# Performance work log

Measured on AMD Instinct MI355X. Metric: run time of the kernel, lower is better.

The kernel has to match this reference:

```python
import jax, jax.numpy as jnp
import numpy as np

T_STEP, NUM_PATCHES = 16, 49
DIM, MLP_DIM, HEADS, DEPTH = 512, 2048, 8, 4
PATCH_DIM = 432
N_BATCH = 32
NEG = -1e9
EPS = 1e-5


def _ln(x, g, b):
    m = x.mean(-1, keepdims=True)
    v = ((x - m) ** 2).mean(-1, keepdims=True)
    return (x - m) / jnp.sqrt(v + EPS) * g + b


def setup_inputs() -> dict:
    key = jax.random.key(0)
    ks = jax.random.split(key, 16)
    L = T_STEP * NUM_PATCHES
    s = 0.02
    return {
        "patch": jax.random.normal(ks[0], (N_BATCH, L, PATCH_DIM), jnp.float32),
        "done": jax.random.randint(ks[1], (N_BATCH, T_STEP - 1), 0, 2).astype(jnp.int32),
        "W_embed": jax.random.normal(ks[2], (PATCH_DIM, DIM), jnp.float32) * s,
        "b_embed": jnp.zeros((DIM,), jnp.float32),
        "spatial_embed": jax.random.normal(ks[3], (1, NUM_PATCHES, DIM), jnp.float32),
        "temporal_embed": jax.random.normal(ks[4], (1, T_STEP, DIM), jnp.float32),
        "ln1_g": jnp.ones((DEPTH, DIM), jnp.float32),
        "ln1_b": jnp.zeros((DEPTH, DIM), jnp.float32),
        "Wqkv": jax.random.normal(ks[5], (DEPTH, DIM, 3 * DIM), jnp.float32) * s,
        "bqkv": jnp.zeros((DEPTH, 3 * DIM), jnp.float32),
        "Wo": jax.random.normal(ks[6], (DEPTH, DIM, DIM), jnp.float32) * s,
        "bo": jnp.zeros((DEPTH, DIM), jnp.float32),
        "ln2_g": jnp.ones((DEPTH, DIM), jnp.float32),
        "ln2_b": jnp.zeros((DEPTH, DIM), jnp.float32),
        "W1": jax.random.normal(ks[7], (DEPTH, DIM, MLP_DIM), jnp.float32) * s,
        "b1": jnp.zeros((DEPTH, MLP_DIM), jnp.float32),
        "W2": jax.random.normal(ks[8], (DEPTH, MLP_DIM, DIM), jnp.float32) * s,
        "b2": jnp.zeros((DEPTH, DIM), jnp.float32),
        "out_g": jnp.ones((DIM,), jnp.float32),
        "out_b": jnp.zeros((DIM,), jnp.float32),
    }


def reference(patch, done, W_embed, b_embed, spatial_embed, temporal_embed,
              ln1_g, ln1_b, Wqkv, bqkv, Wo, bo, ln2_g, ln2_b,
              W1, b1, W2, b2, out_g, out_b):
    N, L, _ = patch.shape
    # patch embed + factored pos embed
    x = patch @ W_embed + b_embed
    pos = jnp.tile(spatial_embed, (1, T_STEP, 1)) + jnp.repeat(temporal_embed, NUM_PATCHES, axis=1)
    x = x + pos
    # episodic attention mask: done_mask[n,t] = 1 iff any done[n, c]==1 for c >= t
    d = done.astype(jnp.float32)  # (N, T-1)
    dm = (jnp.flip(jnp.cumsum(jnp.flip(d, 1), 1), 1) > 0).astype(jnp.float32)
    dm = jnp.concatenate([dm, jnp.zeros((N, 1), jnp.float32)], axis=1)  # (N, T)
    pm = jnp.repeat(dm, NUM_PATCHES, axis=1)  # (N, L)
    keep = 1.0 - pm
    mask = 1.0 - keep[:, :, None] * keep[:, None, :]  # (N, L, L); 1 = blocked
    bias = jnp.where(mask > 0.5, NEG, 0.0)[:, None, :, :]  # (N, 1, L, L)
    dh = DIM // HEADS
    scale = dh ** -0.5
    for i in range(DEPTH):
        h = _ln(x, ln1_g[i], ln1_b[i])
        qkv = h @ Wqkv[i] + bqkv[i]
        q, k, v = jnp.split(qkv, 3, axis=-1)
        q = q.reshape(N, L, HEADS, dh).transpose(0, 2, 1, 3)
        k = k.reshape(N, L, HEADS, dh).transpose(0, 2, 1, 3)
        v = v.reshape(N, L, HEADS, dh).transpose(0, 2, 1, 3)
        scores = jnp.einsum('nhqd,nhkd->nhqk', q, k) * scale + bias
        attn = jax.nn.softmax(scores, axis=-1)
        o = jnp.einsum('nhqk,nhkd->nhqd', attn, v)
        o = o.transpose(0, 2, 1, 3).reshape(N, L, DIM)
        x = x + (o @ Wo[i] + bo[i])
        h = _ln(x, ln2_g[i], ln2_b[i])
        x = x + (jax.nn.gelu(h @ W1[i] + b1[i], approximate=False) @ W2[i] + b2[i])
    return _ln(x, out_g, out_b)
```

## Files before the change

kernel.cpp:

```cpp
#include <hip/hip_runtime.h>
#include <math.h>

#define NB 32
#define LQ 784
#define LQP 832
#define DIM 512
#define HEADS 8
#define MLP 2048
#define KPAD 448
#define MROWS 25088

typedef __attribute__((ext_vector_type(8))) short s8v;
typedef __attribute__((ext_vector_type(4))) short s4v;
typedef __attribute__((ext_vector_type(4))) float f4v;

__device__ __forceinline__ short f2b(float f){
  unsigned u = __builtin_bit_cast(unsigned, f);
  u = (u + 0x7fffu + ((u >> 16) & 1u)) >> 16;
  return (short)u;
}
__device__ __forceinline__ float b2f(short s){
  unsigned u = ((unsigned)(unsigned short)s) << 16;
  return __builtin_bit_cast(float, u);
}

__device__ __forceinline__ void gll16(const short* g, short* l){
  __builtin_amdgcn_global_load_lds(
      (const __attribute__((address_space(1))) void*)g,
      (__attribute__((address_space(3))) void*)l, 16, 0, 0);
}

__device__ __forceinline__ void xcd_remap(int &bm, int &bn, int gx, int gy){
  int nwg = gx * gy;
  int flat = bm * gx + bn;
  int xcd = flat & 7, idx = flat >> 3;
  int q = nwg >> 3, r = nwg & 7;
  int nf = (xcd < r ? xcd * (q + 1) : r * (q + 1) + (xcd - r) * q) + idx;
  bm = nf / gx;
  bn = nf - bm * gx;
}

__global__ __launch_bounds__(512) void mask_k(const int* __restrict__ done, float* __restrict__ keepL,
                                              int* __restrict__ kmask, int* __restrict__ liveg){
  __shared__ float keep[32][16];
  int tid = threadIdx.x;
  { int n = tid >> 4, t = tid & 15;
    int any = 0;
    for (int c = t; c < 15; ++c) any |= done[n*15 + c];
    keep[n][t] = any ? 0.f : 1.f; }
  __syncthreads();
  for (int i = tid; i < NB*LQP; i += 512){
    int n = i / LQP, l = i - n*LQP;
    keepL[i] = (l < LQ) ? keep[n][l/49] : 0.f;
  }
  if (tid < 32){
    int n = tid, m = 0;
    for (int kb = 0; kb < 13; ++kb){
      int t0 = (kb*64)/49, t1 = (kb*64 + 63)/49; if (t1 > 15) t1 = 15;
      float a = 0.f;
      for (int t = t0; t <= t1; ++t) a += keep[n][t];
      if (a > 0.5f) m |= 1 << kb;
    }
    kmask[n] = m;
  }
  for (int g = tid; g < 392; g += 512){
    float a = 0.f;
    for (int i2 = 0; i2 < 64; ++i2){
      int row = g*64 + i2;
      int n = row / 784, l = row - n*784;
      a += keep[n][l/49];
    }
    liveg[g] = a > 0.5f ? 1 : 0;
  }
}

__global__ __launch_bounds__(256) void zpad_k(short* __restrict__ Qb, short* __restrict__ Kb,
                                              short* __restrict__ Vtb){
  int idx = blockIdx.x*256 + threadIdx.x;
  s8v z;
  #pragma unroll
  for (int e=0;e<8;++e) z[e] = 0;
  if (idx < 98304){
    int nh = idx / 384, r = idx - nh*384;
    *(s8v*)(Qb + (long)nh*LQP*64 + 784*64 + r*8) = z;
  } else if (idx < 196608){
    int i2 = idx - 98304; int nh = i2 / 384, r = i2 - nh*384;
    *(s8v*)(Kb + (long)nh*LQP*64 + 784*64 + r*8) = z;
  } else {
    int i2 = idx - 196608; int nh = i2 / 384, rem = i2 - nh*384, d = rem/6, s = rem - d*6;
    *(s8v*)(Vtb + ((long)nh*64 + d)*LQP + 784 + s*8) = z;
  }
}

__global__ __launch_bounds__(256) void vmean_k(const short* __restrict__ Vtb, float* __restrict__ Vm){
  int nh = blockIdx.x;
  int tid = threadIdx.x;
  int d = tid >> 2, seg = tid & 3;
  const short* row = Vtb + ((long)nh*64 + d)*LQP;
  float s = 0.f;
  for (int c = seg; c < 98; c += 4){
    s8v v = *(const s8v*)(row + c*8);
    #pragma unroll
    for (int e=0;e<8;++e) s += b2f(v[e]);
  }
  s += __shfl_xor(s, 1, 64);
  s += __shfl_xor(s, 2, 64);
  if (seg == 0) Vm[nh*64 + d] = s * (1.0f/784.0f);
}

#define PB0 5488
__global__ __launch_bounds__(256) void prep_k(
    const float* __restrict__ patch, short* __restrict__ patchb){
  int unit = blockIdx.x*256 + threadIdx.x;
  int r = unit / 56, c8 = unit - r*56;
  s8v o;
  if (c8 < 54){
    const float* src = patch + (long)r*432 + c8*8;
    float4 a = *(const float4*)src;
    float4 b = *(const float4*)(src + 4);
    o[0]=f2b(a.x); o[1]=f2b(a.y); o[2]=f2b(a.z); o[3]=f2b(a.w);
    o[4]=f2b(b.x); o[5]=f2b(b.y); o[6]=f2b(b.z); o[7]=f2b(b.w);
  } else {
    #pragma unroll
    for (int e=0;e<8;++e) o[e] = 0;
  }
  *(s8v*)(patchb + (long)r*KPAD + c8*8) = o;
}

__device__ __forceinline__ void tile_tr(const float* __restrict__ src, short* __restrict__ dst,
                                        int R, int C, int Rpad, int tr, int tc, int tid,
                                        float (*tile)[65]){
  int r0 = tr*64, c0 = tc*64;
  int w = tid >> 6, lane = tid & 63;
  #pragma unroll
  for (int p = 0; p < 16; ++p){
    int r = r0 + p*4 + w;
    tile[p*4 + w][lane] = (r < R) ? src[(long)r*C + c0 + lane] : 0.f;
  }
  __syncthreads();
  #pragma unroll
  for (int p = 0; p < 16; ++p){
    int cc = p*4 + w;
    dst[(long)(c0 + cc)*Rpad + r0 + lane] = f2b(tile[lane][cc]);
  }
}

__global__ __launch_bounds__(256) void trans_k(
    const float* __restrict__ Wemb, short* __restrict__ Wembt,
    const float* __restrict__ Wqkv, short* __restrict__ Wqkvt,
    const float* __restrict__ Wo,  short* __restrict__ Wot,
    const float* __restrict__ W1,  short* __restrict__ W1t,
    const float* __restrict__ W2,  short* __restrict__ W2t){
  __shared__ float tile[64][65];
  int b = blockIdx.x, tid = threadIdx.x;
  if (b < 56){
    int tr = b >> 3, tc = b & 7;
    tile_tr(Wemb, Wembt, 432, 512, 448, tr, tc, tid, tile);
  } else if (b < 56 + 768){
    int i = b - 56; int z = i / 192, rem = i - z*192;
    int tr = rem / 24, tc = rem - tr*24;
    tile_tr(Wqkv + (long)z*512*1536, Wqkvt + (long)z*1536*512, 512, 1536, 512, tr, tc, tid, tile);
  } else if (b < 56 + 768 + 256){
    int i = b - 824; int z = i >> 6, rem = i & 63;
    int tr = rem >> 3, tc = rem & 7;
    tile_tr(Wo + (long)z*512*512, Wot + (long)z*512*512, 512, 512, 512, tr, tc, tid, tile);
  } else if (b < 56 + 768 + 256 + 1024){
    int i = b - 1080; int z = i >> 8, rem = i & 255;
    int tr = rem >> 5, tc = rem & 31;
    tile_tr(W1 + (long)z*512*2048, W1t + (long)z*2048*512, 512, 2048, 512, tr, tc, tid, tile);
  } else {
    int i = b - 2104; int z = i >> 8, rem = i & 255;
    int tr = rem >> 3, tc = rem & 7;
    tile_tr(W2 + (long)z*2048*512, W2t + (long)z*512*2048, 2048, 512, 2048, tr, tc, tid, tile);
  }
}

__global__ __launch_bounds__(256) void ln_k(const float* __restrict__ x, const float* __restrict__ g,
                                            const float* __restrict__ b, short* __restrict__ outb,
                                            float* __restrict__ outf){
  int lane = threadIdx.x & 63;
  long row = (long)blockIdx.x * 4 + (threadIdx.x >> 6);
  const float* xr = x + row * DIM + lane * 8;
  float va[8];
  { float4 t0 = *(const float4*)xr; float4 t1 = *(const float4*)(xr + 4);
    va[0]=t0.x; va[1]=t0.y; va[2]=t0.z; va[3]=t0.w;
    va[4]=t1.x; va[5]=t1.y; va[6]=t1.z; va[7]=t1.w; }
  float s = 0.f, q = 0.f;
  #pragma unroll
  for (int j=0;j<8;++j){ s += va[j]; q += va[j]*va[j]; }
  #pragma unroll
  for (int m=1;m<64;m<<=1){ s += __shfl_xor(s,m,64); q += __shfl_xor(q,m,64); }
  float mean = s * (1.0f/DIM);
  float var = q * (1.0f/DIM) - mean*mean;
  float inv = rsqrtf(var + 1e-5f);
  int cb = lane*8;
  if (outb){
    s8v o;
    #pragma unroll
    for (int j=0;j<8;++j) o[j] = f2b((va[j]-mean)*inv*g[cb+j] + b[cb+j]);
    *(s8v*)(outb + row*DIM + cb) = o;
  } else {
    float4 t0, t1;
    t0.x=(va[0]-mean)*inv*g[cb+0]+b[cb+0]; t0.y=(va[1]-mean)*inv*g[cb+1]+b[cb+1];
    t0.z=(va[2]-mean)*inv*g[cb+2]+b[cb+2]; t0.w=(va[3]-mean)*inv*g[cb+3]+b[cb+3];
    t1.x=(va[4]-mean)*inv*g[cb+4]+b[cb+4]; t1.y=(va[5]-mean)*inv*g[cb+5]+b[cb+5];
    t1.z=(va[6]-mean)*inv*g[cb+6]+b[cb+6]; t1.w=(va[7]-mean)*inv*g[cb+7]+b[cb+7];
    *(float4*)(outf + row*DIM + cb) = t0;
    *(float4*)(outf + row*DIM + cb + 4) = t1;
  }
}

template<int EPI>
__global__ __launch_bounds__(256) void gemm_k(
    const short* __restrict__ A, const short* __restrict__ Bt,
    const float* __restrict__ bias, int K, int N,
    float* __restrict__ xres, short* __restrict__ outb,
    const float* __restrict__ sp, const float* __restrict__ tp,
    short* __restrict__ Qb, short* __restrict__ Kb, short* __restrict__ Vtb,
    const int* __restrict__ liveg)
{
  __shared__ __align__(16) short lA[2][128*64];
  __shared__ __align__(16) short lB[2][128*64];
  int bm = blockIdx.y, bn = blockIdx.x;
  xcd_remap(bm, bn, gridDim.x, gridDim.y);
  if (EPI == 1){
    if (bn < 8 && liveg[2*bm] == 0 && liveg[2*bm+1] == 0) return;
  }
  int tid = threadIdx.x;
  int lane = tid & 63, wid = tid >> 6;
  int col = lane & 15, quad = lane >> 4;
  int wm = (wid >> 1) * 64, wn = (wid & 1) * 64;
  f4v acc[4][4];
  #pragma unroll
  for (int i=0;i<4;++i)
    #pragma unroll
    for (int j=0;j<4;++j)
      #pragma unroll
      for (int e=0;e<4;++e) acc[i][j][e] = 0.0f;
  const short* Abase = A + (long)bm*128*K;
  const short* Bbase = Bt + (long)bn*128*K;
  int nt = K >> 6;
  #pragma unroll
  for (int c = 0; c < 4; ++c){
    int v = c*256 + tid;
    int r = v >> 3, j = v & 7;
    int kc = (j ^ (r & 7)) * 8;
    gll16(Abase + (long)r*K + kc, lA[0] + v*8);
    gll16(Bbase + (long)r*K + kc, lB[0] + v*8);
  }
  for (int t = 0; t < nt; ++t){
    int cur = t & 1;
    __builtin_amdgcn_s_barrier();
    __builtin_amdgcn_sched_barrier(0);
    if (t + 1 < nt){
      int kt = (t + 1) << 6;
      #pragma unroll
      for (int c = 0; c < 4; ++c){
        int v = c*256 + tid;
        int r = v >> 3, j = v & 7;
        int kc = (j ^ (r & 7)) * 8;
        gll16(Abase + (long)r*K + kt + kc, lA[cur^1] + v*8);
        gll16(Bbase + (long)r*K + kt + kc, lB[cur^1] + v*8);
      }
      asm volatile("s_waitcnt vmcnt(8)" ::: "memory");
    } else {
      asm volatile("s_waitcnt vmcnt(0)" ::: "memory");
    }
    __builtin_amdgcn_s_barrier();
    __builtin_amdgcn_sched_barrier(0);
    __builtin_amdgcn_s_setprio(1);
    #pragma unroll
    for (int ks = 0; ks < 2; ++ks){
      s8v af[4], bf[4];
      #pragma unroll
      for (int j=0;j<4;++j)
        af[j] = *(const s8v*)&lA[cur][(wm + j*16 + col)*64 + (((ks*4+quad) ^ (col&7)))*8];
      #pragma unroll
      for (int i=0;i<4;++i)
        bf[i] = *(const s8v*)&lB[cur][(wn + i*16 + col)*64 + (((ks*4+quad) ^ (col&7)))*8];
      #pragma unroll
      for (int i=0;i<4;++i)
        #pragma unroll
        for (int j=0;j<4;++j)
          acc[i][j] = __builtin_amdgcn_mfma_f32_16x16x32_bf16(bf[i], af[j], acc[i][j], 0, 0, 0);
    }
    __builtin_amdgcn_s_setprio(0);
    __builtin_amdgcn_sched_barrier(0);
  }
  if (EPI == 1 && bn >= 8){
    __syncthreads();
    short* scr = &lA[0][0];
    #pragma unroll
    for (int i=0;i<4;++i){
      int dl = wn + i*16 + quad*4;
      int gc0 = bn*128 + dl;
      float4 b4 = *(const float4*)(bias + gc0);
      #pragma unroll
      for (int j=0;j<4;++j){
        int ll = wm + j*16 + col;
        scr[(dl+0)*128 + ll] = f2b(acc[i][j][0] + b4.x);
        scr[(dl+1)*128 + ll] = f2b(acc[i][j][1] + b4.y);
        scr[(dl+2)*128 + ll] = f2b(acc[i][j][2] + b4.z);
        scr[(dl+3)*128 + ll] = f2b(acc[i][j][3] + b4.w);
      }
    }
    __syncthreads();
    #pragma unroll
    for (int u=0;u<8;++u){
      int unit = u*256 + tid;
      int d = unit >> 4, c = unit & 15;
      int grow0 = bm*128 + c*8;
      int n2 = grow0 / LQ, l2 = grow0 - n2*LQ;
      int hh = (bn - 8)*2 + (d >> 6);
      long row = ((long)(n2*HEADS + hh))*64 + (d & 63);
      *(s8v*)(Vtb + row*LQP + l2) = *(const s8v*)&scr[d*128 + c*8];
    }
    return;
  }
  #pragma unroll
  for (int j=0;j<4;++j){
    int grow = (int)bm*128 + wm + j*16 + col;
    int l = 0, t = 0, p = 0, n = 0;
    if (EPI == 0){ l = grow % LQ; t = l / 49; p = l - t*49; }
    if (EPI == 1){ n = grow / LQ; l = grow - n*LQ; }
    #pragma unroll
    for (int i=0;i<4;++i){
      int gc0 = (int)bn*128 + wn + i*16 + quad*4;
      float4 b4 = *(const float4*)(bias + gc0);
      float v0 = acc[i][j][0] + b4.x;
      float v1 = acc[i][j][1] + b4.y;
      float v2 = acc[i][j][2] + b4.z;
      float v3 = acc[i][j][3] + b4.w;
      if (EPI == 0){
        float4 s4 = *(const float4*)(sp + p*DIM + gc0);
        float4 t4 = *(const float4*)(tp + t*DIM + gc0);
        float4 o; o.x = v0 + s4.x + t4.x; o.y = v1 + s4.y + t4.y;
        o.z = v2 + s4.z + t4.z; o.w = v3 + s4.w + t4.w;
        *(float4*)(xres + (long)grow*DIM + gc0) = o;
      } else if (EPI == 1){
        if (gc0 < 512){
          int hh = gc0 >> 6, d0 = gc0 & 63;
          s4v o; o[0]=f2b(v0); o[1]=f2b(v1); o[2]=f2b(v2); o[3]=f2b(v3);
          *(s4v*)(Qb + (((long)(n*HEADS + hh))*LQP + l)*64 + d0) = o;
        } else {
          int c2 = gc0 - 512; int hh = c2 >> 6, d0 = c2 & 63;
          s4v o; o[0]=f2b(v0); o[1]=f2b(v1); o[2]=f2b(v2); o[3]=f2b(v3);
          *(s4v*)(Kb + (((long)(n*HEADS + hh))*LQP + l)*64 + d0) = o;
        }
      } else if (EPI == 2){
        float4 xo = *(const float4*)(xres + (long)grow*DIM + gc0);
        xo.x += v0; xo.y += v1; xo.z += v2; xo.w += v3;
        *(float4*)(xres + (long)grow*DIM + gc0) = xo;
      } else if (EPI == 3){
        float g0 = v0 / (1.0f + __expf(-1.595769122f * v0 * (1.0f + 0.044715f*v0*v0)));
        float g1 = v1 / (1.0f + __expf(-1.595769122f * v1 * (1.0f + 0.044715f*v1*v1)));
        float g2 = v2 / (1.0f + __expf(-1.595769122f * v2 * (1.0f + 0.044715f*v2*v2)));
        float g3 = v3 / (1.0f + __expf(-1.595769122f * v3 * (1.0f + 0.044715f*v3*v3)));
        s4v o; o[0]=f2b(g0); o[1]=f2b(g1); o[2]=f2b(g2); o[3]=f2b(g3);
        *(s4v*)(outb + (long)grow*MLP + gc0) = o;
      }
    }
  }
}

__global__ __launch_bounds__(256) void attn_k(
    const short* __restrict__ Qb, const short* __restrict__ Kb,
    const short* __restrict__ Vtb, const float* __restrict__ keepL,
    const int* __restrict__ kmask, const float* __restrict__ Vm,
    short* __restrict__ Ob)
{
  __shared__ __align__(16) short lK[64*64];
  __shared__ __align__(16) short lV[64*64];
  __shared__ __align__(16) short lP[4][16*72];
  int tid = threadIdx.x;
  int lane = tid & 63, wid = tid >> 6;
  int col = lane & 15, quad = lane >> 4;
  int qb = blockIdx.x, h = blockIdx.y, n = blockIdx.z;
  long nh = (long)n*HEADS + h;
  int smask = kmask[n];
  int qr0 = qb*64 + wid*16;
  float vmv[4];
  #pragma unroll
  for (int j=0;j<4;++j) vmv[j] = Vm[nh*64 + j*16 + col];

  if (!((smask >> qb) & 1)){
    #pragma unroll
    for (int j=0;j<4;++j){
      short ov = f2b(vmv[j]);
      #pragma unroll
      for (int r=0;r<4;++r){
        int l = qr0 + quad*4 + r;
        if (l < LQ) Ob[((long)n*LQ + l)*DIM + h*64 + j*16 + col] = ov;
      }
    }
    return;
  }

  const float* kl = keepL + n*LQP;
  const short* qp = Qb + (nh*LQP + qr0 + col)*64 + quad*8;
  s8v aq0 = *(const s8v*)qp;
  s8v aq1 = *(const s8v*)(qp + 32);
  float keepA = kl[qr0 + col];
  if (keepA < 0.5f){
    #pragma unroll
    for (int e=0;e<8;++e){ aq0[e] = 0; aq1[e] = 0; }
  }
  float keepQ[4];
  #pragma unroll
  for (int r=0;r<4;++r) keepQ[r] = kl[qr0 + quad*4 + r];
  float kqs = keepQ[0] + keepQ[1] + keepQ[2] + keepQ[3];
  bool wlive = __ballot(kqs > 0.5f) != 0ull;
  float lsum[4] = {0.f,0.f,0.f,0.f};
  f4v Oacc[4];
  #pragma unroll
  for (int j=0;j<4;++j)
    #pragma unroll
    for (int e=0;e<4;++e) Oacc[j][e] = 0.0f;

  for (int kb = 0; kb < 13; ++kb){
    if (!((smask >> kb) & 1)) continue;
    int kbase = kb*64;
    __syncthreads();
    #pragma unroll
    for (int c = 0; c < 2; ++c){
      int v = c*256 + tid;
      int r = v >> 3, j = v & 7;
      int kc = (j ^ (r & 7)) * 8;
      gll16(Kb + (nh*LQP + kbase + r)*64 + kc, lK + v*8);
    }
    #pragma unroll
    for (int c = 0; c < 2; ++c){
      int v = c*256 + tid;
      int d = v >> 3, j = v & 7;
      int c8 = (j ^ (d & 7)) * 8;
      gll16(Vtb + (nh*64 + d)*LQP + kbase + c8, lV + v*8);
    }
    __syncthreads();
    if (!wlive) continue;
    float pm[4][4];
    #pragma unroll
    for (int ct = 0; ct < 4; ++ct){
      float keepK = kl[kbase + ct*16 + col];
      f4v s;
      #pragma unroll
      for (int e=0;e<4;++e) s[e] = 0.0f;
      #pragma unroll
      for (int ks = 0; ks < 2; ++ks){
        s8v bk = *(const s8v*)&lK[(ct*16 + col)*64 + (((ks*4+quad) ^ (col&7)))*8];
        if (keepK < 0.5f){
          #pragma unroll
          for (int e=0;e<8;++e) bk[e] = 0;
        }
        s = __builtin_amdgcn_mfma_f32_16x16x32_bf16(ks ? aq1 : aq0, bk, s, 0, 0, 0);
      }
      #pragma unroll
      for (int r=0;r<4;++r){
        float a = keepQ[r] * keepK;
        float t = fmaf(s[r], 0.125f, 10000.0f);
        float p = __expf(fmaf(a, t, -10000.0f));
        pm[ct][r] = p;
        lsum[r] += p;
      }
    }
    #pragma unroll
    for (int ct=0; ct<4; ++ct)
      #pragma unroll
      for (int r=0;r<4;++r)
        lP[wid][(quad*4 + r)*72 + ct*16 + col] = f2b(pm[ct][r]);
    #pragma unroll
    for (int j=0;j<4;++j){
      #pragma unroll
      for (int ks=0; ks<2; ++ks){
        s8v ap = *(const s8v*)&lP[wid][col*72 + ks*32 + quad*8];
        s8v bv = *(const s8v*)&lV[(j*16 + col)*64 + (((ks*4+quad) ^ (col&7)))*8];
        Oacc[j] = __builtin_amdgcn_mfma_f32_16x16x32_bf16(ap, bv, Oacc[j], 0, 0, 0);
      }
    }
  }
  #pragma unroll
  for (int m=1; m<16; m<<=1){
    #pragma unroll
    for (int r=0;r<4;++r) lsum[r] += __shfl_xor(lsum[r], m, 64);
  }
  float invl[4];
  #pragma unroll
  for (int r=0;r<4;++r) invl[r] = 1.0f / lsum[r];
  #pragma unroll
  for (int j=0;j<4;++j)
    #pragma unroll
    for (int r=0;r<4;++r){
      int l = qr0 + quad*4 + r;
      if (l < LQ){
        float val = keepQ[r] > 0.5f ? Oacc[j][r] * invl[r] : vmv[j];
        Ob[((long)n*LQ + l)*DIM + h*64 + j*16 + col] = f2b(val);
      }
    }
}

extern "C" void kernel_launch(void* const* d_in, const int* in_sizes, int n_in,
                              void* d_out, int out_size, void* d_ws, size_t ws_size,
                              hipStream_t stream) {
  const float* patch    = (const float*)d_in[0];
  const int*   done     = (const int*)d_in[1];
  const float* W_embed  = (const float*)d_in[2];
  const float* b_embed  = (const float*)d_in[3];
  const float* spatial  = (const float*)d_in[4];
  const float* temporal = (const float*)d_in[5];
  const float* ln1_g    = (const float*)d_in[6];
  const float* ln1_b    = (const float*)d_in[7];
  const float* Wqkv     = (const float*)d_in[8];
  const float* bqkv     = (const float*)d_in[9];
  const float* Wo       = (const float*)d_in[10];
  const float* bo       = (const float*)d_in[11];
  const float* ln2_g    = (const float*)d_in[12];
  const float* ln2_b    = (const float*)d_in[13];
  const float* W1       = (const float*)d_in[14];
  const float* b1       = (const float*)d_in[15];
  const float* W2       = (const float*)d_in[16];
  const float* b2       = (const float*)d_in[17];
  const float* out_g    = (const float*)d_in[18];
  const float* out_b    = (const float*)d_in[19];
  float* out = (float*)d_out;

  char* ws = (char*)d_ws;
  size_t off = 0;
  auto alloc = [&](size_t bytes)->char*{ char* p = ws + off; off += (bytes + 255) & ~(size_t)255; return p; };
  const size_t QKV_B = (size_t)NB*HEADS*LQP*64*2;
  float* x    = (float*)alloc((size_t)MROWS*DIM*4);
  short* hbuf = (short*)alloc((size_t)MROWS*DIM*2);
  char*  U    = alloc((size_t)MROWS*MLP*2);
  short* patchb = (short*)U;
  short* Qb   = (short*)U;
  short* Kbf  = (short*)(U + QKV_B);
  short* Vtb  = (short*)(U + 2*QKV_B);
  short* obuf = hbuf;
  short* mid  = (short*)U;
  short* Wembt = (short*)alloc((size_t)512*448*2);
  short* Wqkvt = (short*)alloc((size_t)4*1536*512*2);
  short* Wot   = (short*)alloc((size_t)4*512*512*2);
  short* W1t   = (short*)alloc((size_t)4*2048*512*2);
  short* W2t   = (short*)alloc((size_t)4*512*2048*2);
  float* keepL = (float*)alloc((size_t)NB*LQP*4);
  int*   kmask = (int*)alloc(NB*4);
  int*   liveg = (int*)alloc(392*4);
  float* Vm    = (float*)alloc((size_t)NB*HEADS*64*4);

  mask_k<<<1, 512, 0, stream>>>(done, keepL, kmask, liveg);
  prep_k<<<PB0, 256, 0, stream>>>(patch, patchb);
  trans_k<<<3128, 256, 0, stream>>>(W_embed, Wembt, Wqkv, Wqkvt, Wo, Wot, W1, W1t, W2, W2t);

  gemm_k<0><<<dim3(DIM/128, MROWS/128), 256, 0, stream>>>(
      patchb, Wembt, b_embed, KPAD, DIM, x, nullptr, spatial, temporal,
      nullptr, nullptr, nullptr, nullptr);

  zpad_k<<<1152, 256, 0, stream>>>(Qb, Kbf, Vtb);

  for (int i = 0; i < 4; ++i){
    ln_k<<<MROWS/4, 256, 0, stream>>>(x, ln1_g + i*DIM, ln1_b + i*DIM, hbuf, nullptr);
    gemm_k<1><<<dim3(1536/128, MROWS/128), 256, 0, stream>>>(
        hbuf, Wqkvt + (size_t)i*1536*512, bqkv + (size_t)i*1536, DIM, 1536,
        nullptr, nullptr, nullptr, nullptr, Qb, Kbf, Vtb, liveg);
    vmean_k<<<NB*HEADS, 256, 0, stream>>>(Vtb, Vm);
    attn_k<<<dim3(13, HEADS, NB), 256, 0, stream>>>(Qb, Kbf, Vtb, keepL, kmask, Vm, obuf);
    gemm_k<2><<<dim3(DIM/128, MROWS/128), 256, 0, stream>>>(
        obuf, Wot + (size_t)i*512*512, bo + (size_t)i*DIM, DIM, DIM,
        x, nullptr, nullptr, nullptr, nullptr, nullptr, nullptr, nullptr);
    ln_k<<<MROWS/4, 256, 0, stream>>>(x, ln2_g + i*DIM, ln2_b + i*DIM, hbuf, nullptr);
    gemm_k<3><<<dim3(MLP/128, MROWS/128), 256, 0, stream>>>(
        hbuf, W1t + (size_t)i*2048*512, b1 + (size_t)i*MLP, DIM, MLP,
        nullptr, mid, nullptr, nullptr, nullptr, nullptr, nullptr, nullptr);
    gemm_k<2><<<dim3(DIM/128, MROWS/128), 256, 0, stream>>>(
        mid, W2t + (size_t)i*512*2048, b2 + (size_t)i*DIM, MLP, DIM,
        x, nullptr, nullptr, nullptr, nullptr, nullptr, nullptr, nullptr);
  }
  ln_k<<<MROWS/4, 256, 0, stream>>>(x, out_g, out_b, nullptr, out);
}
```

Measured before the change: 1.488 ms.

## Fold layernorm into GEMM epilogues via gamma-scaled weights and per-row stats

Folds LayerNorm gamma into the transposed QKV and W1 weights and precomputes per-column correction vectors (the column sums of gamma*W and beta*W plus bias). The residual-writing GEMMs now also write a bf16 copy of x, and a light stats kernel computes per-row mean and rstd from it. The QKV and W1 GEMMs then consume raw bf16 x and apply the normalization in the epilogue. This removes the normalized-activation write and reread of the full LN passes. In exchange it adds an extra bf16 store per residual update and computes the statistics from the bf16 copy, which changes numerics slightly.

```diff
diff --git a/kernel.cpp b/kernel.cpp
--- a/kernel.cpp
+++ b/kernel.cpp
@@ -129,13 +129,14 @@
 
 __device__ __forceinline__ void tile_tr(const float* __restrict__ src, short* __restrict__ dst,
                                         int R, int C, int Rpad, int tr, int tc, int tid,
-                                        float (*tile)[65]){
+                                        float (*tile)[65], const float* __restrict__ g){
   int r0 = tr*64, c0 = tc*64;
   int w = tid >> 6, lane = tid & 63;
   #pragma unroll
   for (int p = 0; p < 16; ++p){
     int r = r0 + p*4 + w;
-    tile[p*4 + w][lane] = (r < R) ? src[(long)r*C + c0 + lane] : 0.f;
+    float gv = (g && r < R) ? g[r] : 1.f;
+    tile[p*4 + w][lane] = (r < R) ? gv * src[(long)r*C + c0 + lane] : 0.f;
   }
   __syncthreads();
   #pragma unroll
@@ -150,34 +151,87 @@
     const float* __restrict__ Wqkv, short* __restrict__ Wqkvt,
     const float* __restrict__ Wo,  short* __restrict__ Wot,
     const float* __restrict__ W1,  short* __restrict__ W1t,
-    const float* __restrict__ W2,  short* __restrict__ W2t){
+    const float* __restrict__ W2,  short* __restrict__ W2t,
+    const float* __restrict__ ln1_g, const float* __restrict__ ln2_g){
   __shared__ float tile[64][65];
   int b = blockIdx.x, tid = threadIdx.x;
   if (b < 56){
     int tr = b >> 3, tc = b & 7;
-    tile_tr(Wemb, Wembt, 432, 512, 448, tr, tc, tid, tile);
+    tile_tr(Wemb, Wembt, 432, 512, 448, tr, tc, tid, tile, nullptr);
   } else if (b < 56 + 768){
     int i = b - 56; int z = i / 192, rem = i - z*192;
     int tr = rem / 24, tc = rem - tr*24;
-    tile_tr(Wqkv + (long)z*512*1536, Wqkvt + (long)z*1536*512, 512, 1536, 512, tr, tc, tid, tile);
+    tile_tr(Wqkv + (long)z*512*1536, Wqkvt + (long)z*1536*512, 512, 1536, 512, tr, tc, tid, tile,
+            ln1_g + z*512);
   } else if (b < 56 + 768 + 256){
     int i = b - 824; int z = i >> 6, rem = i & 63;
     int tr = rem >> 3, tc = rem & 7;
-    tile_tr(Wo + (long)z*512*512, Wot + (long)z*512*512, 512, 512, 512, tr, tc, tid, tile);
+    tile_tr(Wo + (long)z*512*512, Wot + (long)z*512*512, 512, 512, 512, tr, tc, tid, tile, nullptr);
   } else if (b < 56 + 768 + 256 + 1024){
     int i = b - 1080; int z = i >> 8, rem = i & 255;
     int tr = rem >> 5, tc = rem & 31;
-    tile_tr(W1 + (long)z*512*2048, W1t + (long)z*2048*512, 512, 2048, 512, tr, tc, tid, tile);
+    tile_tr(W1 + (long)z*512*2048, W1t + (long)z*2048*512, 512, 2048, 512, tr, tc, tid, tile,
+            ln2_g + z*512);
   } else {
     int i = b - 2104; int z = i >> 8, rem = i & 255;
     int tr = rem >> 3, tc = rem & 7;
-    tile_tr(W2 + (long)z*2048*512, W2t + (long)z*512*2048, 2048, 512, 2048, tr, tc, tid, tile);
+    tile_tr(W2 + (long)z*2048*512, W2t + (long)z*512*2048, 2048, 512, 2048, tr, tc, tid, tile, nullptr);
+  }
+}
+
+__global__ __launch_bounds__(256) void cvec_k(
+    const float* __restrict__ Wqkv, const float* __restrict__ bqkv,
+    const float* __restrict__ ln1_g, const float* __restrict__ ln1_b,
+    const float* __restrict__ W1, const float* __restrict__ b1,
+    const float* __restrict__ ln2_g, const float* __restrict__ ln2_b,
+    float* __restrict__ c1qkv, float* __restrict__ cbqkv,
+    float* __restrict__ c1w1, float* __restrict__ cbw1){
+  int b = blockIdx.x, tid = threadIdx.x;
+  if (b < 24){
+    int z = b / 6, n = (b - z*6)*256 + tid;
+    const float* W = Wqkv + (long)z*512*1536;
+    const float* g = ln1_g + z*512; const float* bb = ln1_b + z*512;
+    float c1 = 0.f, c2 = 0.f;
+    #pragma unroll 4
+    for (int k = 0; k < 512; ++k){
+      float w = W[(long)k*1536 + n];
+      c1 += g[k]*w; c2 += bb[k]*w;
+    }
+    c1qkv[z*1536 + n] = c1;
+    cbqkv[z*1536 + n] = c2 + bqkv[z*1536 + n];
+  } else {
+    int i = b - 24; int z = i / 8, n = (i - z*8)*256 + tid;
+    const float* W = W1 + (long)z*512*2048;
+    const float* g = ln2_g + z*512; const float* bb = ln2_b + z*512;
+    float c1 = 0.f, c2 = 0.f;
+    #pragma unroll 4
+    for (int k = 0; k < 512; ++k){
+      float w = W[(long)k*2048 + n];
+      c1 += g[k]*w; c2 += bb[k]*w;
+    }
+    c1w1[z*2048 + n] = c1;
+    cbw1[z*2048 + n] = c2 + b1[z*2048 + n];
+  }
+}
+
+__global__ __launch_bounds__(256) void stats_k(const short* __restrict__ xb, float2* __restrict__ mi){
+  int lane = threadIdx.x & 63;
+  long row = (long)blockIdx.x * 4 + (threadIdx.x >> 6);
+  s8v v = *(const s8v*)(xb + row*DIM + lane*8);
+  float s = 0.f, q = 0.f;
+  #pragma unroll
+  for (int e=0;e<8;++e){ float f = b2f(v[e]); s += f; q += f*f; }
+  #pragma unroll
+  for (int m=1;m<64;m<<=1){ s += __shfl_xor(s,m,64); q += __shfl_xor(q,m,64); }
+  if (lane == 0){
+    float m = s * (1.0f/DIM);
+    float var = q * (1.0f/DIM) - m*m;
+    mi[row] = make_float2(m, rsqrtf(var + 1e-5f));
   }
 }
 
 __global__ __launch_bounds__(256) void ln_k(const float* __restrict__ x, const float* __restrict__ g,
-                                            const float* __restrict__ b, short* __restrict__ outb,
-                                            float* __restrict__ outf){
+                                            const float* __restrict__ b, float* __restrict__ outf){
   int lane = threadIdx.x & 63;
   long row = (long)blockIdx.x * 4 + (threadIdx.x >> 6);
   const float* xr = x + row * DIM + lane * 8;
@@ -194,20 +248,13 @@
   float var = q * (1.0f/DIM) - mean*mean;
   float inv = rsqrtf(var + 1e-5f);
   int cb = lane*8;
-  if (outb){
-    s8v o;
-    #pragma unroll
-    for (int j=0;j<8;++j) o[j] = f2b((va[j]-mean)*inv*g[cb+j] + b[cb+j]);
-    *(s8v*)(outb + row*DIM + cb) = o;
-  } else {
-    float4 t0, t1;
-    t0.x=(va[0]-mean)*inv*g[cb+0]+b[cb+0]; t0.y=(va[1]-mean)*inv*g[cb+1]+b[cb+1];
-    t0.z=(va[2]-mean)*inv*g[cb+2]+b[cb+2]; t0.w=(va[3]-mean)*inv*g[cb+3]+b[cb+3];
-    t1.x=(va[4]-mean)*inv*g[cb+4]+b[cb+4]; t1.y=(va[5]-mean)*inv*g[cb+5]+b[cb+5];
-    t1.z=(va[6]-mean)*inv*g[cb+6]+b[cb+6]; t1.w=(va[7]-mean)*inv*g[cb+7]+b[cb+7];
-    *(float4*)(outf + row*DIM + cb) = t0;
-    *(float4*)(outf + row*DIM + cb + 4) = t1;
-  }
+  float4 t0, t1;
+  t0.x=(va[0]-mean)*inv*g[cb+0]+b[cb+0]; t0.y=(va[1]-mean)*inv*g[cb+1]+b[cb+1];
+  t0.z=(va[2]-mean)*inv*g[cb+2]+b[cb+2]; t0.w=(va[3]-mean)*inv*g[cb+3]+b[cb+3];
+  t1.x=(va[4]-mean)*inv*g[cb+4]+b[cb+4]; t1.y=(va[5]-mean)*inv*g[cb+5]+b[cb+5];
+  t1.z=(va[6]-mean)*inv*g[cb+6]+b[cb+6]; t1.w=(va[7]-mean)*inv*g[cb+7]+b[cb+7];
+  *(float4*)(outf + row*DIM + cb) = t0;
+  *(float4*)(outf + row*DIM + cb + 4) = t1;
 }
 
 template<int EPI>
@@ -217,7 +264,9 @@
     float* __restrict__ xres, short* __restrict__ outb,
     const float* __restrict__ sp, const float* __restrict__ tp,
     short* __restrict__ Qb, short* __restrict__ Kb, short* __restrict__ Vtb,
-    const int* __restrict__ liveg)
+    const int* __restrict__ liveg,
+    const float2* __restrict__ mi, const float* __restrict__ c1v,
+    short* __restrict__ xb)
 {
   __shared__ __align__(16) short lA[2][128*64];
   __shared__ __align__(16) short lB[2][128*64];
@@ -290,18 +339,23 @@
   if (EPI == 1 && bn >= 8){
     __syncthreads();
     short* scr = &lA[0][0];
+    float2 mvv[4];
+    #pragma unroll
+    for (int j=0;j<4;++j) mvv[j] = mi[bm*128 + wm + j*16 + col];
     #pragma unroll
     for (int i=0;i<4;++i){
       int dl = wn + i*16 + quad*4;
       int gc0 = bn*128 + dl;
-      float4 b4 = *(const float4*)(bias + gc0);
+      float4 c14 = *(const float4*)(c1v + gc0);
+      float4 cb4 = *(const float4*)(bias + gc0);
       #pragma unroll
       for (int j=0;j<4;++j){
         int ll = wm + j*16 + col;
-        scr[(dl+0)*128 + ll] = f2b(acc[i][j][0] + b4.x);
-        scr[(dl+1)*128 + ll] = f2b(acc[i][j][1] + b4.y);
-        scr[(dl+2)*128 + ll] = f2b(acc[i][j][2] + b4.z);
-        scr[(dl+3)*128 + ll] = f2b(acc[i][j][3] + b4.w);
+        float s = mvv[j].y, tc = -mvv[j].x*mvv[j].y;
+        scr[(dl+0)*128 + ll] = f2b(s*acc[i][j][0] + tc*c14.x + cb4.x);
+        scr[(dl+1)*128 + ll] = f2b(s*acc[i][j][1] + tc*c14.y + cb4.y);
+        scr[(dl+2)*128 + ll] = f2b(s*acc[i][j][2] + tc*c14.z + cb4.z);
+        scr[(dl+3)*128 + ll] = f2b(s*acc[i][j][3] + tc*c14.w + cb4.w);
       }
     }
     __syncthreads();
@@ -323,20 +377,33 @@
     int l = 0, t = 0, p = 0, n = 0;
     if (EPI == 0){ l = grow % LQ; t = l / 49; p = l - t*49; }
     if (EPI == 1){ n = grow / LQ; l = grow - n*LQ; }
+    float s = 1.f, tc = 0.f;
+    if (EPI == 1 || EPI == 3){ float2 mv = mi[grow]; s = mv.y; tc = -mv.x*mv.y; }
     #pragma unroll
     for (int i=0;i<4;++i){
       int gc0 = (int)bn*128 + wn + i*16 + quad*4;
       float4 b4 = *(const float4*)(bias + gc0);
-      float v0 = acc[i][j][0] + b4.x;
-      float v1 = acc[i][j][1] + b4.y;
-      float v2 = acc[i][j][2] + b4.z;
-      float v3 = acc[i][j][3] + b4.w;
+      float v0, v1, v2, v3;
+      if (EPI == 1 || EPI == 3){
+        float4 c14 = *(const float4*)(c1v + gc0);
+        v0 = s*acc[i][j][0] + tc*c14.x + b4.x;
+        v1 = s*acc[i][j][1] + tc*c14.y + b4.y;
+        v2 = s*acc[i][j][2] + tc*c14.z + b4.z;
+        v3 = s*acc[i][j][3] + tc*c14.w + b4.w;
+      } else {
+        v0 = acc[i][j][0] + b4.x;
+        v1 = acc[i][j][1] + b4.y;
+        v2 = acc[i][j][2] + b4.z;
+        v3 = acc[i][j][3] + b4.w;
+      }
       if (EPI == 0){
         float4 s4 = *(const float4*)(sp + p*DIM + gc0);
         float4 t4 = *(const float4*)(tp + t*DIM + gc0);
         float4 o; o.x = v0 + s4.x + t4.x; o.y = v1 + s4.y + t4.y;
         o.z = v2 + s4.z + t4.z; o.w = v3 + s4.w + t4.w;
         *(float4*)(xres + (long)grow*DIM + gc0) = o;
+        s4v xo4; xo4[0]=f2b(o.x); xo4[1]=f2b(o.y); xo4[2]=f2b(o.z); xo4[3]=f2b(o.w);
+        *(s4v*)(xb + (long)grow*DIM + gc0) = xo4;
       } else if (EPI == 1){
         if (gc0 < 512){
           int hh = gc0 >> 6, d0 = gc0 & 63;
@@ -351,6 +418,8 @@
         float4 xo = *(const float4*)(xres + (long)grow*DIM + gc0);
         xo.x += v0; xo.y += v1; xo.z += v2; xo.w += v3;
         *(float4*)(xres + (long)grow*DIM + gc0) = xo;
+        s4v xo4; xo4[0]=f2b(xo.x); xo4[1]=f2b(xo.y); xo4[2]=f2b(xo.z); xo4[3]=f2b(xo.w);
+        *(s4v*)(xb + (long)grow*DIM + gc0) = xo4;
       } else if (EPI == 3){
         float g0 = v0 / (1.0f + __expf(-1.595769122f * v0 * (1.0f + 0.044715f*v0*v0)));
         float g1 = v1 / (1.0f + __expf(-1.595769122f * v1 * (1.0f + 0.044715f*v1*v1)));
@@ -527,6 +596,7 @@
   auto alloc = [&](size_t bytes)->char*{ char* p = ws + off; off += (bytes + 255) & ~(size_t)255; return p; };
   const size_t QKV_B = (size_t)NB*HEADS*LQP*64*2;
   float* x    = (float*)alloc((size_t)MROWS*DIM*4);
+  short* xb   = (short*)alloc((size_t)MROWS*DIM*2);
   short* hbuf = (short*)alloc((size_t)MROWS*DIM*2);
   char*  U    = alloc((size_t)MROWS*MLP*2);
   short* patchb = (short*)U;
@@ -544,34 +614,46 @@
   int*   kmask = (int*)alloc(NB*4);
   int*   liveg = (int*)alloc(392*4);
   float* Vm    = (float*)alloc((size_t)NB*HEADS*64*4);
+  float2* mi   = (float2*)alloc((size_t)MROWS*8);
+  float* c1qkv = (float*)alloc((size_t)4*1536*4);
+  float* cbqkv = (float*)alloc((size_t)4*1536*4);
+  float* c1w1  = (float*)alloc((size_t)4*2048*4);
+  float* cbw1  = (float*)alloc((size_t)4*2048*4);
 
   mask_k<<<1, 512, 0, stream>>>(done, keepL, kmask, liveg);
   prep_k<<<PB0, 256, 0, stream>>>(patch, patchb);
-  trans_k<<<3128, 256, 0, stream>>>(W_embed, Wembt, Wqkv, Wqkvt, Wo, Wot, W1, W1t, W2, W2t);
+  trans_k<<<3128, 256, 0, stream>>>(W_embed, Wembt, Wqkv, Wqkvt, Wo, Wot, W1, W1t, W2, W2t,
+                                    ln1_g, ln2_g);
+  cvec_k<<<56, 256, 0, stream>>>(Wqkv, bqkv, ln1_g, ln1_b, W1, b1, ln2_g, ln2_b,
+                                 c1qkv, cbqkv, c1w1, cbw1);
 
   gemm_k<0><<<dim3(DIM/128, MROWS/128), 256, 0, stream>>>(
       patchb, Wembt, b_embed, KPAD, DIM, x, nullptr, spatial, temporal,
-      nullptr, nullptr, nullptr, nullptr);
+      nullptr, nullptr, nullptr, nullptr, nullptr, nullptr, xb);
 
   zpad_k<<<1152, 256, 0, stream>>>(Qb, Kbf, Vtb);
 
   for (int i = 0; i < 4; ++i){
-    ln_k<<<MROWS/4, 256, 0, stream>>>(x, ln1_g + i*DIM, ln1_b + i*DIM, hbuf, nullptr);
+    stats_k<<<MROWS/4, 256, 0, stream>>>(xb, mi);
     gemm_k<1><<<dim3(1536/128, MROWS/128), 256, 0, stream>>>(
-        hbuf, Wqkvt + (size_t)i*1536*512, bqkv + (size_t)i*1536, DIM, 1536,
-        nullptr, nullptr, nullptr, nullptr, Qb, Kbf, Vtb, liveg);
+        xb, Wqkvt + (size_t)i*1536*512, cbqkv + (size_t)i*1536, DIM, 1536,
+        nullptr, nullptr, nullptr, nullptr, Qb, Kbf, Vtb, liveg,
+        mi, c1qkv + (size_t)i*1536, nullptr);
     vmean_k<<<NB*HEADS, 256, 0, stream>>>(Vtb, Vm);
     attn_k<<<dim3(13, HEADS, NB), 256, 0, stream>>>(Qb, Kbf, Vtb, keepL, kmask, Vm, obuf);
     gemm_k<2><<<dim3(DIM/128, MROWS/128), 256, 0, stream>>>(
         obuf, Wot + (size_t)i*512*512, bo + (size_t)i*DIM, DIM, DIM,
-        x, nullptr, nullptr, nullptr, nullptr, nullptr, nullptr, nullptr);
-    ln_k<<<MROWS/4, 256, 0, stream>>>(x, ln2_g + i*DIM, ln2_b + i*DIM, hbuf, nullptr);
+        x, nullptr, nullptr, nullptr, nullptr, nullptr, nullptr, nullptr,
+        nullptr, nullptr, xb);
+    stats_k<<<MROWS/4, 256, 0, stream>>>(xb, mi);
     gemm_k<3><<<dim3(MLP/128, MROWS/128), 256, 0, stream>>>(
-        hbuf, W1t + (size_t)i*2048*512, b1 + (size_t)i*MLP, DIM, MLP,
-        nullptr, mid, nullptr, nullptr, nullptr, nullptr, nullptr, nullptr);
+        xb, W1t + (size_t)i*2048*512, cbw1 + (size_t)i*2048, DIM, MLP,
+        nullptr, mid, nullptr, nullptr, nullptr, nullptr, nullptr, nullptr,
+        mi, c1w1 + (size_t)i*2048, nullptr);
     gemm_k<2><<<dim3(DIM/128, MROWS/128), 256, 0, stream>>>(
         mid, W2t + (size_t)i*512*2048, b2 + (size_t)i*DIM, MLP, DIM,
-        x, nullptr, nullptr, nullptr, nullptr, nullptr, nullptr, nullptr);
-  }
-  ln_k<<<MROWS/4, 256, 0, stream>>>(x, out_g, out_b, nullptr, out);
-}
+        x, nullptr, nullptr, nullptr, nullptr, nullptr, nullptr, nullptr,
+        nullptr, nullptr, xb);
+  }
+  ln_k<<<MROWS/4, 256, 0, stream>>>(x, out_g, out_b, out);
+}
```

New measurement: 1.538 ms. 3.4% more time.
